# Optimization experiments

Hardware: AMD Instinct MI355X
Metric: run time of the kernel (lower is better)

## Reference

```python
import jax, jax.numpy as jnp
import numpy as np

B, S, D, E = 8, 1024, 768, 8
F = 4 * D  # 3072


def setup_inputs() -> dict:
    key = jax.random.key(0)
    ks = jax.random.split(key, 5)
    scale = 0.02
    x = jax.random.normal(ks[0], (B, S, D), jnp.float32)
    gate_w = jax.random.normal(ks[1], (D, E), jnp.float32) * scale
    gate_b = jnp.zeros((E,), jnp.float32)
    w1 = jax.random.normal(ks[2], (E, D, F), jnp.float32) * scale
    b1 = jnp.zeros((E, F), jnp.float32)
    w2 = jax.random.normal(ks[3], (E, F, D), jnp.float32) * scale
    b2 = jnp.zeros((E, D), jnp.float32)
    return {"x": x, "gate_w": gate_w, "gate_b": gate_b,
            "w1": w1, "b1": b1, "w2": w2, "b2": b2}


def reference(x, gate_w, gate_b, w1, b1, w2, b2):
    # x: [B, S, D] -> tokens [T, D]
    orig_shape = x.shape
    xt = x.reshape(-1, x.shape[-1])  # [T, D]
    gates = jax.nn.softmax(xt @ gate_w + gate_b, axis=-1)  # [T, E]
    # original takes topk(k=2) but only uses indices[:, 0] == argmax (top-1)
    expert_idx = jnp.argmax(gates, axis=-1)  # [T]
    # NOTE: original does NOT scale expert output by gate probability.
    out = jnp.zeros_like(xt)
    n_experts = w1.shape[0]
    for e in range(n_experts):  # small fixed expert loop
        h = jax.nn.gelu(xt @ w1[e] + b1[e], approximate=False)  # [T, F]
        y = h @ w2[e] + b2[e]  # [T, D]
        out = jnp.where((expert_idx == e)[:, None], y, out)
    return out.reshape(orig_shape)
```

## Files before the change

kernel.cpp:

```cpp
#include <hip/hip_runtime.h>
#include <hip/hip_bf16.h>
#include <cstdint>
#include <cstddef>

static constexpr int T_TOK = 8192;
static constexpr int D_DIM = 768;
static constexpr int E_NUM = 8;
static constexpr int F_DIM = 3072;
static constexpr int MAX_TILES = 72;

typedef __attribute__((ext_vector_type(8))) short short8;
typedef __attribute__((ext_vector_type(4))) float floatx4;
typedef __attribute__((ext_vector_type(8))) unsigned short ushort8v;

__device__ __forceinline__ void async16(const void* g, void* l) {
  __builtin_amdgcn_global_load_lds(
      (const __attribute__((address_space(1))) unsigned int*)g,
      (__attribute__((address_space(3))) unsigned int*)l, 16, 0, 0);
}

__device__ __forceinline__ float gelu_fast(float v) {
  float s = v * (1.5957691f + 0.071354813f * v * v);
  return v / (1.0f + __expf(-s));
}

__global__ __launch_bounds__(256)
void gate_kernel(const float* __restrict__ x, const float* __restrict__ gw,
                 const float* __restrict__ gb, int* __restrict__ expert_idx,
                 __hip_bfloat16* __restrict__ xb) {
  int gid = blockIdx.x * blockDim.x + threadIdx.x;
  int tok = gid >> 6;
  int lane = threadIdx.x & 63;
  if (tok >= T_TOK) return;
  const float* xr = x + (size_t)tok * D_DIM;
  __hip_bfloat16* xbr = xb + (size_t)tok * D_DIM;
  float acc[8];
#pragma unroll
  for (int e = 0; e < 8; e++) acc[e] = 0.f;
#pragma unroll
  for (int i = 0; i < D_DIM / 64; i++) {
    int d = lane + i * 64;
    float v = xr[d];
    xbr[d] = __float2bfloat16(v);
    const float4* g4 = (const float4*)(gw + (size_t)d * 8);
    float4 a = g4[0], b = g4[1];
    acc[0] += v * a.x; acc[1] += v * a.y; acc[2] += v * a.z; acc[3] += v * a.w;
    acc[4] += v * b.x; acc[5] += v * b.y; acc[6] += v * b.z; acc[7] += v * b.w;
  }
#pragma unroll
  for (int e = 0; e < 8; e++) {
#pragma unroll
    for (int o = 32; o > 0; o >>= 1) acc[e] += __shfl_xor(acc[e], o, 64);
  }
  if (lane == 0) {
    int best = 0;
    float bv = acc[0] + gb[0];
#pragma unroll
    for (int e = 1; e < 8; e++) {
      float v = acc[e] + gb[e];
      if (v > bv) { bv = v; best = e; }
    }
    expert_idx[tok] = best;
  }
}

__global__ __launch_bounds__(256)
void count_kernel(const int* __restrict__ expert_idx, int* __restrict__ counts) {
  __shared__ int h[E_NUM];
  if (threadIdx.x < E_NUM) h[threadIdx.x] = 0;
  __syncthreads();
  int t = blockIdx.x * blockDim.x + threadIdx.x;
  if (t < T_TOK) atomicAdd(&h[expert_idx[t]], 1);
  __syncthreads();
  if (threadIdx.x < E_NUM && h[threadIdx.x] > 0)
    atomicAdd(&counts[threadIdx.x], h[threadIdx.x]);
}

__global__ void offsets_kernel(const int* __restrict__ counts, int* __restrict__ offs,
                               int* __restrict__ meta) {
  if (threadIdx.x == 0) {
    int s = 0, tc = 0;
    for (int e = 0; e < E_NUM; e++) {
      offs[e] = s;
      int cnt = counts[e];
      for (int m = 0; m * 128 < cnt; m++) {
        meta[1 + tc] = e;
        meta[1 + MAX_TILES + tc] = m;
        tc++;
      }
      s += cnt;
    }
    offs[E_NUM] = s;
    meta[0] = tc;
  }
}

__global__ __launch_bounds__(256)
void scatter_kernel(const int* __restrict__ expert_idx, const int* __restrict__ offs,
                    int* __restrict__ fill, int* __restrict__ perm) {
  __shared__ int lcnt[E_NUM];
  __shared__ int lbase[E_NUM];
  if (threadIdx.x < E_NUM) lcnt[threadIdx.x] = 0;
  __syncthreads();
  int t = blockIdx.x * blockDim.x + threadIdx.x;
  int e = -1, rank = 0;
  if (t < T_TOK) {
    e = expert_idx[t];
    rank = atomicAdd(&lcnt[e], 1);
  }
  __syncthreads();
  if (threadIdx.x < E_NUM)
    lbase[threadIdx.x] = (lcnt[threadIdx.x] > 0)
                           ? atomicAdd(&fill[threadIdx.x], lcnt[threadIdx.x]) : 0;
  __syncthreads();
  if (t < T_TOK) perm[offs[e] + lbase[e] + rank] = t;
}

__global__ __launch_bounds__(256)
void transpose_bf16(const float* __restrict__ in, __hip_bfloat16* __restrict__ out,
                    int R, int C) {
  __shared__ float t[64][65];
  const float* src = in + (size_t)blockIdx.z * R * C;
  __hip_bfloat16* dst = out + (size_t)blockIdx.z * R * C;
  int r0 = blockIdx.y * 64, c0 = blockIdx.x * 64;
  int tx = threadIdx.x & 15;
  int ty = threadIdx.x >> 4;
#pragma unroll
  for (int p = 0; p < 4; p++) {
    int r = ty + p * 16;
    float4 v = *(const float4*)&src[(size_t)(r0 + r) * C + c0 + tx * 4];
    t[tx * 4 + 0][r] = v.x; t[tx * 4 + 1][r] = v.y;
    t[tx * 4 + 2][r] = v.z; t[tx * 4 + 3][r] = v.w;
  }
  __syncthreads();
  int j = threadIdx.x & 7;
#pragma unroll
  for (int p = 0; p < 2; p++) {
    int cc = (threadIdx.x >> 3) + p * 32;
    __align__(16) __hip_bfloat16 tmp[8];
#pragma unroll
    for (int i = 0; i < 8; i++) tmp[i] = __float2bfloat16(t[cc][j * 8 + i]);
    *(ushort8v*)&dst[(size_t)(c0 + cc) * R + r0 + j * 8] = *(const ushort8v*)tmp;
  }
}

__global__ __launch_bounds__(256)
void moe_gemm1(const __hip_bfloat16* __restrict__ A,
               const __hip_bfloat16* __restrict__ Bt,
               const float* __restrict__ bias,
               const int* __restrict__ meta,
               const int* __restrict__ offs,
               const int* __restrict__ perm,
               __hip_bfloat16* __restrict__ H) {
  constexpr int K = D_DIM, N = F_DIM;
  int g = blockIdx.x;
  int xcd = g & 7;
  int j = g >> 3;
  int mt = xcd * 9 + (j % 9);
  int nt = j / 9;
  if (mt >= meta[0]) return;
  int e = meta[1 + mt];
  int m0 = meta[1 + MAX_TILES + mt] * 128;
  int off = offs[e], cnt = offs[e + 1] - off;
  int n0 = nt * 128;

  __shared__ __align__(16) __hip_bfloat16 As[2 * 128 * 32];
  __shared__ __align__(16) __hip_bfloat16 Bs[2 * 128 * 32];

  int tid = threadIdx.x, lane = tid & 63, w = tid >> 6;
  int lr0 = w * 32 + (lane >> 2), lr1 = lr0 + 16;
  int ch = (lane & 3) ^ ((lane >> 3) & 3);

  int r0 = m0 + lr0; if (r0 > cnt - 1) r0 = cnt - 1;
  int r1 = m0 + lr1; if (r1 > cnt - 1) r1 = cnt - 1;
  const __hip_bfloat16* a0 = A + (size_t)perm[off + r0] * K + ch * 8;
  const __hip_bfloat16* a1 = A + (size_t)perm[off + r1] * K + ch * 8;
  const __hip_bfloat16* Bbase = Bt + ((size_t)e * N + n0) * K;
  const __hip_bfloat16* bp0 = Bbase + (size_t)lr0 * K + ch * 8;
  const __hip_bfloat16* bp1 = Bbase + (size_t)lr1 * K + ch * 8;

  int wr = (w >> 1) * 64, wc = (w & 1) * 64;
  int mrow = lane & 15, cq = lane >> 4;
  int aoff[4], boff[4];
#pragma unroll
  for (int i = 0; i < 4; i++) {
    int rr = wr + i * 16 + mrow;
    aoff[i] = rr * 32 + ((cq ^ ((rr >> 1) & 3)) * 8);
    int rb = wc + i * 16 + mrow;
    boff[i] = rb * 32 + ((cq ^ ((rb >> 1) & 3)) * 8);
  }

  floatx4 acc[4][4];
#pragma unroll
  for (int i = 0; i < 4; i++)
#pragma unroll
    for (int jj = 0; jj < 4; jj++) acc[i][jj] = (floatx4){0.f, 0.f, 0.f, 0.f};

  for (int kk = 0; kk < K; kk += 64) {
    __syncthreads();
#pragma unroll
    for (int ks = 0; ks < 2; ks++) {
      int ko = kk + ks * 32;
      async16(a0 + ko, &As[ks * 4096 + (w * 32) * 32]);
      async16(a1 + ko, &As[ks * 4096 + (w * 32 + 16) * 32]);
      async16(bp0 + ko, &Bs[ks * 4096 + (w * 32) * 32]);
      async16(bp1 + ko, &Bs[ks * 4096 + (w * 32 + 16) * 32]);
    }
    __syncthreads();
#pragma unroll
    for (int ks = 0; ks < 2; ks++) {
      short8 af[4], bf[4];
#pragma unroll
      for (int i = 0; i < 4; i++) af[i] = *(const short8*)&As[ks * 4096 + aoff[i]];
#pragma unroll
      for (int i = 0; i < 4; i++) bf[i] = *(const short8*)&Bs[ks * 4096 + boff[i]];
#pragma unroll
      for (int mi = 0; mi < 4; mi++)
#pragma unroll
        for (int ni = 0; ni < 4; ni++)
          acc[mi][ni] = __builtin_amdgcn_mfma_f32_16x16x32_bf16(af[mi], bf[ni], acc[mi][ni], 0, 0, 0);
    }
  }

#pragma unroll
  for (int mi = 0; mi < 4; mi++) {
    int rowl = wr + mi * 16 + (lane >> 4) * 4;
#pragma unroll
    for (int ni = 0; ni < 4; ni++) {
      int col = n0 + wc + ni * 16 + (lane & 15);
      float bia = bias[(size_t)e * N + col];
#pragma unroll
      for (int r = 0; r < 4; r++) {
        int gm = m0 + rowl + r;
        if (gm < cnt)
          H[(size_t)(off + gm) * N + col] = __float2bfloat16(gelu_fast(acc[mi][ni][r] + bia));
      }
    }
  }
}

__global__ __launch_bounds__(256)
void moe_gemm2(const __hip_bfloat16* __restrict__ A,
               const __hip_bfloat16* __restrict__ Bt,
               const float* __restrict__ bias,
               const int* __restrict__ meta,
               const int* __restrict__ offs,
               const int* __restrict__ perm,
               float* __restrict__ Out) {
  constexpr int K = F_DIM, N = D_DIM;
  int g = blockIdx.x;
  int xcd = g & 7;
  int j = g >> 3;
  int mt = xcd * 9 + (j % 9);
  int nt = j / 9;
  if (mt >= meta[0]) return;
  int e = meta[1 + mt];
  int m0 = meta[1 + MAX_TILES + mt] * 128;
  int off = offs[e], cnt = offs[e + 1] - off;
  int n0 = nt * 64;

  __shared__ __align__(16) __hip_bfloat16 As[2 * 128 * 32];
  __shared__ __align__(16) __hip_bfloat16 Bs[2 * 64 * 32];

  int tid = threadIdx.x, lane = tid & 63, w = tid >> 6;
  int lr0 = w * 32 + (lane >> 2), lr1 = lr0 + 16;
  int ch = (lane & 3) ^ ((lane >> 3) & 3);

  int r0 = m0 + lr0; if (r0 > cnt - 1) r0 = cnt - 1;
  int r1 = m0 + lr1; if (r1 > cnt - 1) r1 = cnt - 1;
  const __hip_bfloat16* a0 = A + (size_t)(off + r0) * K + ch * 8;
  const __hip_bfloat16* a1 = A + (size_t)(off + r1) * K + ch * 8;
  int br = w * 16 + (lane >> 2);
  const __hip_bfloat16* bp0 = Bt + ((size_t)e * N + n0 + br) * K + ch * 8;

  int mrow = lane & 15, cq = lane >> 4;
  int aoff[2], boff[4];
#pragma unroll
  for (int i = 0; i < 2; i++) {
    int rr = w * 32 + i * 16 + mrow;
    aoff[i] = rr * 32 + ((cq ^ ((rr >> 1) & 3)) * 8);
  }
#pragma unroll
  for (int i = 0; i < 4; i++) {
    int rb = i * 16 + mrow;
    boff[i] = rb * 32 + ((cq ^ ((rb >> 1) & 3)) * 8);
  }

  floatx4 acc[2][4];
#pragma unroll
  for (int i = 0; i < 2; i++)
#pragma unroll
    for (int jj = 0; jj < 4; jj++) acc[i][jj] = (floatx4){0.f, 0.f, 0.f, 0.f};

  for (int kk = 0; kk < K; kk += 64) {
    __syncthreads();
#pragma unroll
    for (int ks = 0; ks < 2; ks++) {
      int ko = kk + ks * 32;
      async16(a0 + ko, &As[ks * 4096 + (w * 32) * 32]);
      async16(a1 + ko, &As[ks * 4096 + (w * 32 + 16) * 32]);
      async16(bp0 + ko, &Bs[ks * 2048 + (w * 16) * 32]);
    }
    __syncthreads();
#pragma unroll
    for (int ks = 0; ks < 2; ks++) {
      short8 af[2], bf[4];
#pragma unroll
      for (int i = 0; i < 2; i++) af[i] = *(const short8*)&As[ks * 4096 + aoff[i]];
#pragma unroll
      for (int i = 0; i < 4; i++) bf[i] = *(const short8*)&Bs[ks * 2048 + boff[i]];
#pragma unroll
      for (int mi = 0; mi < 2; mi++)
#pragma unroll
        for (int ni = 0; ni < 4; ni++)
          acc[mi][ni] = __builtin_amdgcn_mfma_f32_16x16x32_bf16(af[mi], bf[ni], acc[mi][ni], 0, 0, 0);
    }
  }

#pragma unroll
  for (int mi = 0; mi < 2; mi++) {
    int rowl = w * 32 + mi * 16 + (lane >> 4) * 4;
#pragma unroll
    for (int ni = 0; ni < 4; ni++) {
      int col = n0 + ni * 16 + (lane & 15);
      float bia = bias[(size_t)e * N + col];
#pragma unroll
      for (int r = 0; r < 4; r++) {
        int gm = m0 + rowl + r;
        if (gm < cnt)
          Out[(size_t)perm[off + gm] * N + col] = acc[mi][ni][r] + bia;
      }
    }
  }
}

extern "C" void kernel_launch(void* const* d_in, const int* in_sizes, int n_in,
                              void* d_out, int out_size, void* d_ws, size_t ws_size,
                              hipStream_t stream) {
  const float* x  = (const float*)d_in[0];
  const float* gw = (const float*)d_in[1];
  const float* gb = (const float*)d_in[2];
  const float* w1 = (const float*)d_in[3];
  const float* b1 = (const float*)d_in[4];
  const float* w2 = (const float*)d_in[5];
  const float* b2 = (const float*)d_in[6];
  float* out = (float*)d_out;

  char* ws = (char*)d_ws;
  int* counts = (int*)(ws + 0);
  int* fill   = (int*)(ws + 32);
  int* offs   = (int*)(ws + 64);
  int* meta   = (int*)(ws + 128);
  int* eidx   = (int*)(ws + 1024);
  int* perm   = (int*)(ws + 1024 + 4 * T_TOK);
  size_t off = 1024 + 8 * (size_t)T_TOK;
  __hip_bfloat16* xb  = (__hip_bfloat16*)(ws + off); off += (size_t)T_TOK * D_DIM * 2;
  __hip_bfloat16* w1t = (__hip_bfloat16*)(ws + off); off += (size_t)E_NUM * D_DIM * F_DIM * 2;
  __hip_bfloat16* w2t = (__hip_bfloat16*)(ws + off); off += (size_t)E_NUM * D_DIM * F_DIM * 2;
  __hip_bfloat16* H   = (__hip_bfloat16*)(ws + off); off += (size_t)T_TOK * F_DIM * 2;

  hipMemsetAsync(d_ws, 0, 64, stream);
  gate_kernel<<<T_TOK / 4, 256, 0, stream>>>(x, gw, gb, eidx, xb);
  count_kernel<<<T_TOK / 256, 256, 0, stream>>>(eidx, counts);
  offsets_kernel<<<1, 64, 0, stream>>>(counts, offs, meta);
  scatter_kernel<<<T_TOK / 256, 256, 0, stream>>>(eidx, offs, fill, perm);
  transpose_bf16<<<dim3(F_DIM / 64, D_DIM / 64, E_NUM), 256, 0, stream>>>(w1, w1t, D_DIM, F_DIM);
  transpose_bf16<<<dim3(D_DIM / 64, F_DIM / 64, E_NUM), 256, 0, stream>>>(w2, w2t, F_DIM, D_DIM);
  moe_gemm1<<<8 * 9 * (F_DIM / 128), 256, 0, stream>>>(xb, w1t, b1, meta, offs, perm, H);
  moe_gemm2<<<8 * 9 * (D_DIM / 64), 256, 0, stream>>>(H, w2t, b2, meta, offs, perm, out);
}
```

Measured before the change: 385.6 us.

## Switch expert GEMMs to 32x32x16 MFMA and shrink gemm1 N-tile

Both expert GEMMs move from 16x16x32 to 32x32x16 bf16 MFMA instructions with 16-float accumulators, and each wave now computes a 32x64 output tile. Gemm1's N tile drops from 128 to 64, which doubles its grid, and both kernels gain an occupancy hint of 4 blocks per SIMD. The tile-to-XCD mapping is interleaved so that consecutive M tiles land on different XCDs. The intent is fewer MFMA issues, more resident blocks and better load balance across XCDs, at the cost of less B-tile reuse per block in gemm1 and more A traffic.

```diff
diff --git a/kernel.cpp b/kernel.cpp
--- a/kernel.cpp
+++ b/kernel.cpp
@@ -10,7 +10,7 @@
 static constexpr int MAX_TILES = 72;
 
 typedef __attribute__((ext_vector_type(8))) short short8;
-typedef __attribute__((ext_vector_type(4))) float floatx4;
+typedef __attribute__((ext_vector_type(16))) float floatx16;
 typedef __attribute__((ext_vector_type(8))) unsigned short ushort8v;
 
 __device__ __forceinline__ void async16(const void* g, void* l) {
@@ -144,7 +144,7 @@
   }
 }
 
-__global__ __launch_bounds__(256)
+__global__ __launch_bounds__(256, 4)
 void moe_gemm1(const __hip_bfloat16* __restrict__ A,
                const __hip_bfloat16* __restrict__ Bt,
                const float* __restrict__ bias,
@@ -156,16 +156,16 @@
   int g = blockIdx.x;
   int xcd = g & 7;
   int j = g >> 3;
-  int mt = xcd * 9 + (j % 9);
+  int mt = (j % 9) * 8 + xcd;
   int nt = j / 9;
   if (mt >= meta[0]) return;
   int e = meta[1 + mt];
   int m0 = meta[1 + MAX_TILES + mt] * 128;
   int off = offs[e], cnt = offs[e + 1] - off;
-  int n0 = nt * 128;
+  int n0 = nt * 64;
 
   __shared__ __align__(16) __hip_bfloat16 As[2 * 128 * 32];
-  __shared__ __align__(16) __hip_bfloat16 Bs[2 * 128 * 32];
+  __shared__ __align__(16) __hip_bfloat16 Bs[2 * 64 * 32];
 
   int tid = threadIdx.x, lane = tid & 63, w = tid >> 6;
   int lr0 = w * 32 + (lane >> 2), lr1 = lr0 + 16;
@@ -175,26 +175,28 @@
   int r1 = m0 + lr1; if (r1 > cnt - 1) r1 = cnt - 1;
   const __hip_bfloat16* a0 = A + (size_t)perm[off + r0] * K + ch * 8;
   const __hip_bfloat16* a1 = A + (size_t)perm[off + r1] * K + ch * 8;
-  const __hip_bfloat16* Bbase = Bt + ((size_t)e * N + n0) * K;
-  const __hip_bfloat16* bp0 = Bbase + (size_t)lr0 * K + ch * 8;
-  const __hip_bfloat16* bp1 = Bbase + (size_t)lr1 * K + ch * 8;
-
-  int wr = (w >> 1) * 64, wc = (w & 1) * 64;
-  int mrow = lane & 15, cq = lane >> 4;
-  int aoff[4], boff[4];
-#pragma unroll
-  for (int i = 0; i < 4; i++) {
-    int rr = wr + i * 16 + mrow;
-    aoff[i] = rr * 32 + ((cq ^ ((rr >> 1) & 3)) * 8);
-    int rb = wc + i * 16 + mrow;
-    boff[i] = rb * 32 + ((cq ^ ((rb >> 1) & 3)) * 8);
-  }
-
-  floatx4 acc[4][4];
-#pragma unroll
-  for (int i = 0; i < 4; i++)
-#pragma unroll
-    for (int jj = 0; jj < 4; jj++) acc[i][jj] = (floatx4){0.f, 0.f, 0.f, 0.f};
+  int brow = w * 16 + (lane >> 2);
+  const __hip_bfloat16* bp = Bt + ((size_t)e * N + n0 + brow) * K + ch * 8;
+
+  int q = lane >> 5;
+  int row_a = w * 32 + (lane & 31);
+  int aoff[2], boff[2][2];
+#pragma unroll
+  for (int kst = 0; kst < 2; kst++) {
+    int c = kst * 2 + q;
+    aoff[kst] = row_a * 32 + ((c ^ ((row_a >> 1) & 3)) * 8);
+#pragma unroll
+    for (int ni = 0; ni < 2; ni++) {
+      int row_b = ni * 32 + (lane & 31);
+      boff[ni][kst] = row_b * 32 + ((c ^ ((row_b >> 1) & 3)) * 8);
+    }
+  }
+
+  floatx16 acc[2];
+#pragma unroll
+  for (int ni = 0; ni < 2; ni++)
+#pragma unroll
+    for (int i = 0; i < 16; i++) acc[ni][i] = 0.f;
 
   for (int kk = 0; kk < K; kk += 64) {
     __syncthreads();
@@ -203,43 +205,41 @@
       int ko = kk + ks * 32;
       async16(a0 + ko, &As[ks * 4096 + (w * 32) * 32]);
       async16(a1 + ko, &As[ks * 4096 + (w * 32 + 16) * 32]);
-      async16(bp0 + ko, &Bs[ks * 4096 + (w * 32) * 32]);
-      async16(bp1 + ko, &Bs[ks * 4096 + (w * 32 + 16) * 32]);
+      async16(bp + ko, &Bs[ks * 2048 + (w * 16) * 32]);
     }
     __syncthreads();
 #pragma unroll
     for (int ks = 0; ks < 2; ks++) {
-      short8 af[4], bf[4];
-#pragma unroll
-      for (int i = 0; i < 4; i++) af[i] = *(const short8*)&As[ks * 4096 + aoff[i]];
-#pragma unroll
-      for (int i = 0; i < 4; i++) bf[i] = *(const short8*)&Bs[ks * 4096 + boff[i]];
-#pragma unroll
-      for (int mi = 0; mi < 4; mi++)
-#pragma unroll
-        for (int ni = 0; ni < 4; ni++)
-          acc[mi][ni] = __builtin_amdgcn_mfma_f32_16x16x32_bf16(af[mi], bf[ni], acc[mi][ni], 0, 0, 0);
-    }
-  }
-
-#pragma unroll
-  for (int mi = 0; mi < 4; mi++) {
-    int rowl = wr + mi * 16 + (lane >> 4) * 4;
-#pragma unroll
-    for (int ni = 0; ni < 4; ni++) {
-      int col = n0 + wc + ni * 16 + (lane & 15);
-      float bia = bias[(size_t)e * N + col];
-#pragma unroll
-      for (int r = 0; r < 4; r++) {
-        int gm = m0 + rowl + r;
-        if (gm < cnt)
-          H[(size_t)(off + gm) * N + col] = __float2bfloat16(gelu_fast(acc[mi][ni][r] + bia));
+#pragma unroll
+      for (int kst = 0; kst < 2; kst++) {
+        short8 af = *(const short8*)&As[ks * 4096 + aoff[kst]];
+#pragma unroll
+        for (int ni = 0; ni < 2; ni++) {
+          short8 bf = *(const short8*)&Bs[ks * 2048 + boff[ni][kst]];
+          acc[ni] = __builtin_amdgcn_mfma_f32_32x32x16_bf16(af, bf, acc[ni], 0, 0, 0);
+        }
       }
     }
   }
-}
-
-__global__ __launch_bounds__(256)
+
+  int gmr[16];
+#pragma unroll
+  for (int reg = 0; reg < 16; reg++)
+    gmr[reg] = m0 + w * 32 + (reg & 3) + 8 * (reg >> 2) + 4 * q;
+#pragma unroll
+  for (int ni = 0; ni < 2; ni++) {
+    int col = n0 + ni * 32 + (lane & 31);
+    float bia = bias[(size_t)e * N + col];
+#pragma unroll
+    for (int reg = 0; reg < 16; reg++) {
+      if (gmr[reg] < cnt)
+        H[(size_t)(off + gmr[reg]) * N + col] =
+            __float2bfloat16(gelu_fast(acc[ni][reg] + bia));
+    }
+  }
+}
+
+__global__ __launch_bounds__(256, 4)
 void moe_gemm2(const __hip_bfloat16* __restrict__ A,
                const __hip_bfloat16* __restrict__ Bt,
                const float* __restrict__ bias,
@@ -251,7 +251,7 @@
   int g = blockIdx.x;
   int xcd = g & 7;
   int j = g >> 3;
-  int mt = xcd * 9 + (j % 9);
+  int mt = (j % 9) * 8 + xcd;
   int nt = j / 9;
   if (mt >= meta[0]) return;
   int e = meta[1 + mt];
@@ -270,27 +270,28 @@
   int r1 = m0 + lr1; if (r1 > cnt - 1) r1 = cnt - 1;
   const __hip_bfloat16* a0 = A + (size_t)(off + r0) * K + ch * 8;
   const __hip_bfloat16* a1 = A + (size_t)(off + r1) * K + ch * 8;
-  int br = w * 16 + (lane >> 2);
-  const __hip_bfloat16* bp0 = Bt + ((size_t)e * N + n0 + br) * K + ch * 8;
-
-  int mrow = lane & 15, cq = lane >> 4;
-  int aoff[2], boff[4];
-#pragma unroll
-  for (int i = 0; i < 2; i++) {
-    int rr = w * 32 + i * 16 + mrow;
-    aoff[i] = rr * 32 + ((cq ^ ((rr >> 1) & 3)) * 8);
-  }
-#pragma unroll
-  for (int i = 0; i < 4; i++) {
-    int rb = i * 16 + mrow;
-    boff[i] = rb * 32 + ((cq ^ ((rb >> 1) & 3)) * 8);
-  }
-
-  floatx4 acc[2][4];
-#pragma unroll
-  for (int i = 0; i < 2; i++)
-#pragma unroll
-    for (int jj = 0; jj < 4; jj++) acc[i][jj] = (floatx4){0.f, 0.f, 0.f, 0.f};
+  int brow = w * 16 + (lane >> 2);
+  const __hip_bfloat16* bp = Bt + ((size_t)e * N + n0 + brow) * K + ch * 8;
+
+  int q = lane >> 5;
+  int row_a = w * 32 + (lane & 31);
+  int aoff[2], boff[2][2];
+#pragma unroll
+  for (int kst = 0; kst < 2; kst++) {
+    int c = kst * 2 + q;
+    aoff[kst] = row_a * 32 + ((c ^ ((row_a >> 1) & 3)) * 8);
+#pragma unroll
+    for (int ni = 0; ni < 2; ni++) {
+      int row_b = ni * 32 + (lane & 31);
+      boff[ni][kst] = row_b * 32 + ((c ^ ((row_b >> 1) & 3)) * 8);
+    }
+  }
+
+  floatx16 acc[2];
+#pragma unroll
+  for (int ni = 0; ni < 2; ni++)
+#pragma unroll
+    for (int i = 0; i < 16; i++) acc[ni][i] = 0.f;
 
   for (int kk = 0; kk < K; kk += 64) {
     __syncthreads();
@@ -299,37 +300,37 @@
       int ko = kk + ks * 32;
       async16(a0 + ko, &As[ks * 4096 + (w * 32) * 32]);
       async16(a1 + ko, &As[ks * 4096 + (w * 32 + 16) * 32]);
-      async16(bp0 + ko, &Bs[ks * 2048 + (w * 16) * 32]);
+      async16(bp + ko, &Bs[ks * 2048 + (w * 16) * 32]);
     }
     __syncthreads();
 #pragma unroll
     for (int ks = 0; ks < 2; ks++) {
-      short8 af[2], bf[4];
-#pragma unroll
-      for (int i = 0; i < 2; i++) af[i] = *(const short8*)&As[ks * 4096 + aoff[i]];
-#pragma unroll
-      for (int i = 0; i < 4; i++) bf[i] = *(const short8*)&Bs[ks * 2048 + boff[i]];
-#pragma unroll
-      for (int mi = 0; mi < 2; mi++)
-#pragma unroll
-        for (int ni = 0; ni < 4; ni++)
-          acc[mi][ni] = __builtin_amdgcn_mfma_f32_16x16x32_bf16(af[mi], bf[ni], acc[mi][ni], 0, 0, 0);
-    }
-  }
-
-#pragma unroll
-  for (int mi = 0; mi < 2; mi++) {
-    int rowl = w * 32 + mi * 16 + (lane >> 4) * 4;
-#pragma unroll
-    for (int ni = 0; ni < 4; ni++) {
-      int col = n0 + ni * 16 + (lane & 15);
-      float bia = bias[(size_t)e * N + col];
-#pragma unroll
-      for (int r = 0; r < 4; r++) {
-        int gm = m0 + rowl + r;
-        if (gm < cnt)
-          Out[(size_t)perm[off + gm] * N + col] = acc[mi][ni][r] + bia;
+#pragma unroll
+      for (int kst = 0; kst < 2; kst++) {
+        short8 af = *(const short8*)&As[ks * 4096 + aoff[kst]];
+#pragma unroll
+        for (int ni = 0; ni < 2; ni++) {
+          short8 bf = *(const short8*)&Bs[ks * 2048 + boff[ni][kst]];
+          acc[ni] = __builtin_amdgcn_mfma_f32_32x32x16_bf16(af, bf, acc[ni], 0, 0, 0);
+        }
       }
+    }
+  }
+
+  int dst[16];
+#pragma unroll
+  for (int reg = 0; reg < 16; reg++) {
+    int gm = m0 + w * 32 + (reg & 3) + 8 * (reg >> 2) + 4 * q;
+    dst[reg] = (gm < cnt) ? perm[off + gm] : -1;
+  }
+#pragma unroll
+  for (int ni = 0; ni < 2; ni++) {
+    int col = n0 + ni * 32 + (lane & 31);
+    float bia = bias[(size_t)e * N + col];
+#pragma unroll
+    for (int reg = 0; reg < 16; reg++) {
+      if (dst[reg] >= 0)
+        Out[(size_t)dst[reg] * N + col] = acc[ni][reg] + bia;
     }
   }
 }
@@ -366,6 +367,6 @@
   scatter_kernel<<<T_TOK / 256, 256, 0, stream>>>(eidx, offs, fill, perm);
   transpose_bf16<<<dim3(F_DIM / 64, D_DIM / 64, E_NUM), 256, 0, stream>>>(w1, w1t, D_DIM, F_DIM);
   transpose_bf16<<<dim3(D_DIM / 64, F_DIM / 64, E_NUM), 256, 0, stream>>>(w2, w2t, F_DIM, D_DIM);
-  moe_gemm1<<<8 * 9 * (F_DIM / 128), 256, 0, stream>>>(xb, w1t, b1, meta, offs, perm, H);
+  moe_gemm1<<<8 * 9 * (F_DIM / 64), 256, 0, stream>>>(xb, w1t, b1, meta, offs, perm, H);
   moe_gemm2<<<8 * 9 * (D_DIM / 64), 256, 0, stream>>>(H, w2t, b2, meta, offs, perm, out);
 }
```

After: 405.9 us. 1.05x slower.
